# Kernel optimization log

Measured on AMD Instinct MI355X. Metric: run time of the kernel, lower is better.

## Reference

```python
import jax, jax.numpy as jnp
import numpy as np

L, B, E, H = 1024, 8, 1024, 16
HD = E // H
SCALE = HD ** -0.5
EPS = 1e-5


def setup_inputs() -> dict:
    key = jax.random.key(0)
    ks = jax.random.split(key, 6)
    s = E ** -0.5
    return {
        "x": jax.random.normal(ks[0], (L, B, E), dtype=jnp.float32),
        "attn_mask": jnp.zeros((L, L), dtype=jnp.float32),
        "Wq": jax.random.normal(ks[1], (E, E), dtype=jnp.float32) * s,
        "bq": jnp.zeros((E,), dtype=jnp.float32),
        "Wk": jax.random.normal(ks[2], (E, E), dtype=jnp.float32) * s,
        "bk": jnp.zeros((E,), dtype=jnp.float32),
        "Wv": jax.random.normal(ks[3], (E, E), dtype=jnp.float32) * s,
        "bv": jnp.zeros((E,), dtype=jnp.float32),
        "Wo": jax.random.normal(ks[4], (E, E), dtype=jnp.float32) * s,
        "bo": jnp.zeros((E,), dtype=jnp.float32),
        "gamma": jnp.ones((E,), dtype=jnp.float32),
        "beta": jnp.zeros((E,), dtype=jnp.float32),
    }


def _layernorm(x, gamma, beta):
    mu = jnp.mean(x, axis=-1, keepdims=True)
    var = jnp.mean(jnp.square(x - mu), axis=-1, keepdims=True)
    return (x - mu) * jax.lax.rsqrt(var + EPS) * gamma + beta


def reference(x, attn_mask, Wq, bq, Wk, bk, Wv, bv, Wo, bo, gamma, beta):
    # x: (L, B, E); pre-LN residual attention block (dropout=0, eval)
    ln_x = _layernorm(x, gamma, beta)
    # torch Linear: y = x @ W.T + b
    q = (ln_x @ Wq.T + bq) * SCALE
    k = ln_x @ Wk.T + bk
    v = ln_x @ Wv.T + bv
    # (L, B, E) -> (B, H, L, hd)
    def split_heads(t):
        return t.reshape(L, B, H, HD).transpose(1, 2, 0, 3)
    q, k, v = split_heads(q), split_heads(k), split_heads(v)
    # full attention matrix, as in the original non-fused bmm path
    attn = jnp.einsum('bhqd,bhkd->bhqk', q, k) + attn_mask[None, None]
    attn = jax.nn.softmax(attn, axis=-1)
    out = jnp.einsum('bhqk,bhkd->bhqd', attn, v)  # (B, H, L, hd)
    out = out.transpose(2, 0, 1, 3).reshape(L, B, E)
    out = out @ Wo.T + bo
    return x + out
```

## Files before the change

kernel.cpp:

```cpp
#include <hip/hip_runtime.h>

#define LL 1024
#define BB 8
#define EE 1024
#define HH 16
#define HD 64
#define MROWS (LL*BB)

typedef __attribute__((ext_vector_type(8))) short short8v;
typedef __attribute__((ext_vector_type(4))) float f32x4;
typedef __attribute__((ext_vector_type(16))) float f32x16;

#define LOG2E 1.44269504088896f

__device__ __forceinline__ unsigned short tobf(float f) {
    union { float f; unsigned u; } un; un.f = f;
    unsigned u = un.u;
    u += 0x7fffu + ((u >> 16) & 1u);
    return (unsigned short)(u >> 16);
}

__device__ __forceinline__ float max3f(float a, float b, float c) {
    return fmaxf(fmaxf(a, b), c);
}

__device__ __forceinline__ void load_lds16(const unsigned short* g, unsigned short* l) {
    __builtin_amdgcn_global_load_lds((const __attribute__((address_space(1))) unsigned int*)g,
                                     (__attribute__((address_space(3))) unsigned int*)l,
                                     16, 0, 0);
}

__global__ __launch_bounds__(256) void convw4_kernel(const float* __restrict__ w0,
                                                     const float* __restrict__ w1,
                                                     const float* __restrict__ w2,
                                                     const float* __restrict__ w3,
                                                     unsigned short* __restrict__ o0,
                                                     unsigned short* __restrict__ o1,
                                                     unsigned short* __restrict__ o2,
                                                     unsigned short* __restrict__ o3) {
    const float* w; unsigned short* o;
    switch (blockIdx.y) {
        case 0:  w = w0; o = o0; break;
        case 1:  w = w1; o = o1; break;
        case 2:  w = w2; o = o2; break;
        default: w = w3; o = o3; break;
    }
    int i = (blockIdx.x * 256 + threadIdx.x) * 4;
    float4 v = *(const float4*)&w[i];
    ushort4 r;
    r.x = tobf(v.x); r.y = tobf(v.y); r.z = tobf(v.z); r.w = tobf(v.w);
    *(ushort4*)&o[i] = r;
}

__global__ __launch_bounds__(256) void ln_kernel(const float* __restrict__ x,
                                                 const float* __restrict__ gamma,
                                                 const float* __restrict__ beta,
                                                 unsigned short* __restrict__ out) {
    const int row = blockIdx.x;
    const int tid = threadIdx.x;
    const float4 v = *(const float4*)&x[(size_t)row * EE + tid * 4];
    float s = v.x + v.y + v.z + v.w;
    float q = v.x*v.x + v.y*v.y + v.z*v.z + v.w*v.w;
    #pragma unroll
    for (int off = 1; off < 64; off <<= 1) {
        s += __shfl_xor(s, off);
        q += __shfl_xor(q, off);
    }
    __shared__ float ss[4], sq[4];
    const int wv = tid >> 6;
    if ((tid & 63) == 0) { ss[wv] = s; sq[wv] = q; }
    __syncthreads();
    s = ss[0] + ss[1] + ss[2] + ss[3];
    q = sq[0] + sq[1] + sq[2] + sq[3];
    const float mu = s * (1.0f / EE);
    const float var = q * (1.0f / EE) - mu * mu;
    const float rs = rsqrtf(var + 1e-5f);
    ushort4 o;
    o.x = tobf((v.x - mu) * rs * gamma[tid*4+0] + beta[tid*4+0]);
    o.y = tobf((v.y - mu) * rs * gamma[tid*4+1] + beta[tid*4+1]);
    o.z = tobf((v.z - mu) * rs * gamma[tid*4+2] + beta[tid*4+2]);
    o.w = tobf((v.w - mu) * rs * gamma[tid*4+3] + beta[tid*4+3]);
    *(ushort4*)&out[(size_t)row * EE + tid * 4] = o;
}

#define GEMM128_BODY(A_, W_)                                                              \
    __shared__ unsigned short a_sh[128*64];                                               \
    __shared__ unsigned short b_sh[128*64];                                               \
    const int tid = threadIdx.x, lane = tid & 63, wave = tid >> 6;                        \
    const int bm = blockIdx.y * 128, bn = blockIdx.x * 128;                               \
    const int wr = (wave >> 1) * 64, wc = (wave & 1) * 64;                                \
    const int l16 = lane & 15, q4 = lane >> 4;                                            \
    const int grow8 = lane >> 3;                                                          \
    const int gsl = ((lane & 7) ^ grow8) * 8;                                             \
    f32x4 acc[4][4] = {};                                                                 \
    for (int k0 = 0; k0 < EE; k0 += 64) {                                                 \
        _Pragma("unroll")                                                                 \
        for (int i = 0; i < 4; ++i) {                                                     \
            const int ch = wave * 4 + i;                                                  \
            load_lds16(&A_[(size_t)(bm + ch*8 + grow8)*EE + k0 + gsl], a_sh + ch*512);    \
            load_lds16(&W_[(size_t)(bn + ch*8 + grow8)*EE + k0 + gsl], b_sh + ch*512);    \
        }                                                                                 \
        __syncthreads();                                                                  \
        _Pragma("unroll")                                                                 \
        for (int kh = 0; kh < 2; ++kh) {                                                  \
            short8v af[4], bf[4];                                                         \
            _Pragma("unroll")                                                             \
            for (int mi = 0; mi < 4; ++mi)                                                \
                af[mi] = *(const short8v*)((const char*)a_sh                              \
                           + (size_t)(wr + mi*16 + l16)*128 + (((kh*4 + q4) ^ (l16 & 7))*16)); \
            _Pragma("unroll")                                                             \
            for (int ni = 0; ni < 4; ++ni)                                                \
                bf[ni] = *(const short8v*)((const char*)b_sh                              \
                           + (size_t)(wc + ni*16 + l16)*128 + (((kh*4 + q4) ^ (l16 & 7))*16)); \
            _Pragma("unroll")                                                             \
            for (int mi = 0; mi < 4; ++mi)                                                \
                _Pragma("unroll")                                                         \
                for (int ni = 0; ni < 4; ++ni)                                            \
                    acc[mi][ni] = __builtin_amdgcn_mfma_f32_16x16x32_bf16(af[mi], bf[ni], acc[mi][ni], 0, 0, 0); \
        }                                                                                 \
        __syncthreads();                                                                  \
    }

__global__ __launch_bounds__(256) void gemm_qkv(const unsigned short* __restrict__ A,
                                                const unsigned short* __restrict__ W,
                                                const float* __restrict__ bq,
                                                const float* __restrict__ bk,
                                                const float* __restrict__ bv,
                                                unsigned short* __restrict__ qo,
                                                unsigned short* __restrict__ ko,
                                                unsigned short* __restrict__ vo) {
    GEMM128_BODY(A, W)
    const int seg = blockIdx.x >> 3;
    const float* bias = seg == 0 ? bq : (seg == 1 ? bk : bv);
    #pragma unroll
    for (int mi = 0; mi < 4; ++mi) {
        #pragma unroll
        for (int ni = 0; ni < 4; ++ni) {
            #pragma unroll
            for (int r = 0; r < 4; ++r) {
                const int m  = bm + wr + mi*16 + (lane >> 4)*4 + r;
                const int nn = (bn & 1023) + wc + ni*16 + l16;
                const float v = acc[mi][ni][r] + bias[nn];
                const int l = m >> 3, b = m & 7, h = nn >> 6, d = nn & 63;
                if (seg == 0)      qo[((size_t)(b*HH + h) * LL + l) * HD + d] = tobf(v * (0.125f * LOG2E));
                else if (seg == 1) ko[((size_t)(b*HH + h) * LL + l) * HD + d] = tobf(v);
                else               vo[((size_t)(b*HH + h) * HD + d) * LL + l] = tobf(v);
            }
        }
    }
}

__global__ __launch_bounds__(256) void gemm_o(const unsigned short* __restrict__ A,
                                              const unsigned short* __restrict__ W,
                                              const float* __restrict__ bias,
                                              const float* __restrict__ xres,
                                              float* __restrict__ outf) {
    GEMM128_BODY(A, W)
    #pragma unroll
    for (int mi = 0; mi < 4; ++mi) {
        #pragma unroll
        for (int ni = 0; ni < 4; ++ni) {
            #pragma unroll
            for (int r = 0; r < 4; ++r) {
                const int m = bm + wr + mi*16 + (lane >> 4)*4 + r;
                const int n = bn + wc + ni*16 + l16;
                outf[(size_t)m * EE + n] = acc[mi][ni][r] + bias[n] + xres[(size_t)m * EE + n];
            }
        }
    }
}

__global__ __launch_bounds__(256) void attn_kernel(const unsigned short* __restrict__ qarr,
                                                   const unsigned short* __restrict__ karr,
                                                   const unsigned short* __restrict__ vtarr,
                                                   const float* __restrict__ mask,
                                                   unsigned short* __restrict__ attn_out) {
    __shared__ __attribute__((aligned(16))) unsigned short k_sh[2][64*64];
    __shared__ __attribute__((aligned(16))) unsigned short v_sh[2][64*64];
    const int tid = threadIdx.x, lane = tid & 63, wave = tid >> 6;
    const int l32 = lane & 31, hi = lane >> 5;
    const int bh = blockIdx.y;
    const int qtok = blockIdx.x * 128 + wave * 32 + l32;
    const unsigned short* qb = qarr  + (size_t)bh * LL * HD;
    const unsigned short* kb = karr  + (size_t)bh * LL * HD;
    const unsigned short* vb = vtarr + (size_t)bh * HD * LL;

    short8v qf[4];
    #pragma unroll
    for (int dc = 0; dc < 4; ++dc)
        qf[dc] = *(const short8v*)&qb[(size_t)qtok * HD + dc*16 + hi*8];

    f32x16 acc[2] = {};
    float mrun = -1e30f, srun = 0.f;

    auto stage = [&](int buf, int kv) {
        #pragma unroll
        for (int i = 0; i < 2; ++i) {
            const int r = wave*16 + i*8 + (lane >> 3);
            const int c = ((lane & 7) ^ (r & 7)) * 8;
            load_lds16(&kb[(size_t)(kv + r) * HD + c], &k_sh[buf][(wave*16 + i*8) * 64]);
            load_lds16(&vb[(size_t)r * LL + kv + c],   &v_sh[buf][(wave*16 + i*8) * 64]);
        }
    };

    const float* mbase = &mask[(size_t)qtok * LL + hi*4];
    float4 mcur[4], mnxt[4];
    #pragma unroll
    for (int g = 0; g < 4; ++g) mcur[g] = *(const float4*)&mbase[g*8];

    stage(0, 0);
    for (int t = 0; t < LL/64; ++t) {
        const int buf = t & 1;
        __syncthreads();
        if (t < LL/64 - 1) stage(buf ^ 1, (t + 1) * 64);

        #pragma unroll
        for (int sub = 0; sub < 2; ++sub) {
            {
                const int nt = (sub == 0) ? t : (t < LL/64 - 1 ? t + 1 : t);
                const int ns = sub ^ 1;
                const float* mrow = &mbase[(size_t)nt*64 + ns*32];
                #pragma unroll
                for (int g = 0; g < 4; ++g) mnxt[g] = *(const float4*)&mrow[g*8];
            }
            f32x16 s = {};
            __builtin_amdgcn_s_setprio(1);
            #pragma unroll
            for (int dc = 0; dc < 4; ++dc) {
                const int row = sub*32 + l32;
                const short8v kf = *(const short8v*)((const char*)&k_sh[buf][0]
                                     + (size_t)row*128 + (((dc*2 + hi) ^ (l32 & 7)) * 16));
                s = __builtin_amdgcn_mfma_f32_32x32x16_bf16(kf, qf[dc], s, 0, 0, 0);
            }
            __builtin_amdgcn_s_setprio(0);
            #pragma unroll
            for (int g = 0; g < 4; ++g) {
                s[4*g+0] = fmaf(mcur[g].x, LOG2E, s[4*g+0]);
                s[4*g+1] = fmaf(mcur[g].y, LOG2E, s[4*g+1]);
                s[4*g+2] = fmaf(mcur[g].z, LOG2E, s[4*g+2]);
                s[4*g+3] = fmaf(mcur[g].w, LOG2E, s[4*g+3]);
            }
            #pragma unroll
            for (int g = 0; g < 4; ++g) mcur[g] = mnxt[g];
            const float a0 = max3f(s[0],  s[1],  s[2]);
            const float a1 = max3f(s[3],  s[4],  s[5]);
            const float a2 = max3f(s[6],  s[7],  s[8]);
            const float a3 = max3f(s[9],  s[10], s[11]);
            const float a4 = max3f(s[12], s[13], s[14]);
            float pm = fmaxf(max3f(a0, a1, a2), max3f(a3, a4, s[15]));
            pm = fmaxf(pm, __shfl_xor(pm, 32));
            if (__any(pm - mrun > 8.0f)) {
                const float mn = fmaxf(mrun, pm);
                const float al = exp2f(mrun - mn);
                #pragma unroll
                for (int i = 0; i < 16; ++i) { acc[0][i] *= al; acc[1][i] *= al; }
                srun *= al;
                mrun = mn;
            }
            float p[16];
            #pragma unroll
            for (int i = 0; i < 16; ++i) p[i] = exp2f(s[i] - mrun);
            const float t0 = p[0]+p[1],   t1 = p[2]+p[3],   t2 = p[4]+p[5],   t3 = p[6]+p[7];
            const float t4 = p[8]+p[9],   t5 = p[10]+p[11], t6 = p[12]+p[13], t7 = p[14]+p[15];
            const float u0 = t0+t1, u1 = t2+t3, u2 = t4+t5, u3 = t6+t7;
            float rs = (u0+u1) + (u2+u3);
            rs += __shfl_xor(rs, 32);
            srun += rs;
            unsigned w[8];
            #pragma unroll
            for (int j = 0; j < 8; ++j)
                asm("v_cvt_pk_bf16_f32 %0, %1, %2" : "=v"(w[j]) : "v"(p[2*j]), "v"(p[2*j+1]));
            asm volatile("v_permlane32_swap_b32 %0, %1" : "+v"(w[0]), "+v"(w[2]));
            asm volatile("v_permlane32_swap_b32 %0, %1" : "+v"(w[1]), "+v"(w[3]));
            asm volatile("v_permlane32_swap_b32 %0, %1" : "+v"(w[4]), "+v"(w[6]));
            asm volatile("v_permlane32_swap_b32 %0, %1" : "+v"(w[5]), "+v"(w[7]));
            union { uint4 u; short8v s8; } pb0, pb1;
            pb0.u = make_uint4(w[0], w[1], w[2], w[3]);
            pb1.u = make_uint4(w[4], w[5], w[6], w[7]);
            __builtin_amdgcn_s_setprio(1);
            #pragma unroll
            for (int dt = 0; dt < 2; ++dt) {
                const int row = dt*32 + l32;
                const short8v vf0 = *(const short8v*)((const char*)&v_sh[buf][0]
                                      + (size_t)row*128 + ((((sub*2+0)*2 + hi) ^ (l32 & 7)) * 16));
                const short8v vf1 = *(const short8v*)((const char*)&v_sh[buf][0]
                                      + (size_t)row*128 + ((((sub*2+1)*2 + hi) ^ (l32 & 7)) * 16));
                acc[dt] = __builtin_amdgcn_mfma_f32_32x32x16_bf16(vf0, pb0.s8, acc[dt], 0, 0, 0);
                acc[dt] = __builtin_amdgcn_mfma_f32_32x32x16_bf16(vf1, pb1.s8, acc[dt], 0, 0, 0);
            }
            __builtin_amdgcn_s_setprio(0);
        }
    }
    const float inv = 1.0f / srun;
    const int b = bh >> 4, h = bh & 15;
    unsigned short* orow = attn_out + ((size_t)qtok * BB + b) * EE + h * HD;
    #pragma unroll
    for (int dt = 0; dt < 2; ++dt) {
        #pragma unroll
        for (int g = 0; g < 4; ++g) {
            const float a0 = acc[dt][4*g+0]*inv, a1 = acc[dt][4*g+1]*inv;
            const float a2 = acc[dt][4*g+2]*inv, a3 = acc[dt][4*g+3]*inv;
            unsigned lo, hw;
            asm("v_cvt_pk_bf16_f32 %0, %1, %2" : "=v"(lo) : "v"(a0), "v"(a1));
            asm("v_cvt_pk_bf16_f32 %0, %1, %2" : "=v"(hw) : "v"(a2), "v"(a3));
            *(uint2*)&orow[dt*32 + g*8 + hi*4] = make_uint2(lo, hw);
        }
    }
}

extern "C" void kernel_launch(void* const* d_in, const int* in_sizes, int n_in,
                              void* d_out, int out_size, void* d_ws, size_t ws_size,
                              hipStream_t stream) {
    (void)in_sizes; (void)n_in; (void)out_size; (void)ws_size;
    const float* x     = (const float*)d_in[0];
    const float* mask  = (const float*)d_in[1];
    const float* Wq    = (const float*)d_in[2];
    const float* bq    = (const float*)d_in[3];
    const float* Wk    = (const float*)d_in[4];
    const float* bk    = (const float*)d_in[5];
    const float* Wv    = (const float*)d_in[6];
    const float* bv    = (const float*)d_in[7];
    const float* Wo    = (const float*)d_in[8];
    const float* bo    = (const float*)d_in[9];
    const float* gamma = (const float*)d_in[10];
    const float* beta  = (const float*)d_in[11];
    float* out = (float*)d_out;

    unsigned short* ws   = (unsigned short*)d_ws;
    unsigned short* ln   = ws;
    unsigned short* wqkv = ln   + (size_t)MROWS * EE;
    unsigned short* wob  = wqkv + (size_t)3 * EE * EE;
    unsigned short* qb   = wob  + (size_t)EE * EE;
    unsigned short* kbp  = qb   + (size_t)BB * HH * LL * HD;
    unsigned short* vtb  = kbp  + (size_t)BB * HH * LL * HD;
    unsigned short* attnb = ln;

    convw4_kernel<<<dim3(1024, 4), 256, 0, stream>>>(
        Wq, Wk, Wv, Wo,
        wqkv, wqkv + (size_t)EE * EE, wqkv + (size_t)2 * EE * EE, wob);
    ln_kernel<<<MROWS, 256, 0, stream>>>(x, gamma, beta, ln);

    gemm_qkv<<<dim3(24, 64), 256, 0, stream>>>(ln, wqkv, bq, bk, bv, qb, kbp, vtb);

    attn_kernel<<<dim3(LL / 128, BB * HH), 256, 0, stream>>>(qb, kbp, vtb, mask, attnb);

    gemm_o<<<dim3(8, 64), 256, 0, stream>>>(attnb, wob, bo, x, out);
}
```

Baseline: 228.9 us.

## Double-buffer GEMM K-tiles and batch both QK^T sub-tiles before softmax

The shared GEMM body now uses a K step of 32 with two LDS buffers, prefetching the next tile while MFMAs run on the current one, and drops the XOR swizzle in favour of a plain row layout. The attention loop now issues all eight QK^T MFMAs for both 32-key halves up front, then runs softmax and PV on each half through a shared lambda. Mask prefetch across iterations is replaced by loads within the iteration. The unswizzled LDS layout may cause bank conflicts, and holding two score tiles raises register pressure.

```diff
diff --git a/kernel.cpp b/kernel.cpp
--- a/kernel.cpp
+++ b/kernel.cpp
@@ -84,40 +84,41 @@
 }
 
 #define GEMM128_BODY(A_, W_)                                                              \
-    __shared__ unsigned short a_sh[128*64];                                               \
-    __shared__ unsigned short b_sh[128*64];                                               \
+    __shared__ unsigned short a_sh[2][128*32];                                            \
+    __shared__ unsigned short b_sh[2][128*32];                                            \
     const int tid = threadIdx.x, lane = tid & 63, wave = tid >> 6;                        \
     const int bm = blockIdx.y * 128, bn = blockIdx.x * 128;                               \
     const int wr = (wave >> 1) * 64, wc = (wave & 1) * 64;                                \
-    const int l16 = lane & 15, q4 = lane >> 4;                                            \
-    const int grow8 = lane >> 3;                                                          \
-    const int gsl = ((lane & 7) ^ grow8) * 8;                                             \
+    const int l16 = lane & 15, lk8 = (lane >> 4) * 8;                                     \
+    const int grow = lane >> 2, gcol = (lane & 3) * 8;                                    \
     f32x4 acc[4][4] = {};                                                                 \
-    for (int k0 = 0; k0 < EE; k0 += 64) {                                                 \
+    _Pragma("unroll")                                                                     \
+    for (int i = 0; i < 2; ++i) {                                                         \
+        const int ch = wave * 2 + i;                                                      \
+        load_lds16(&A_[(size_t)(bm + ch*16 + grow)*EE + gcol], &a_sh[0][ch*512]);         \
+        load_lds16(&W_[(size_t)(bn + ch*16 + grow)*EE + gcol], &b_sh[0][ch*512]);         \
+    }                                                                                     \
+    __syncthreads();                                                                      \
+    for (int k0 = 0; k0 < EE; k0 += 32) {                                                 \
+        const int cur = (k0 >> 5) & 1;                                                    \
+        if (k0 + 32 < EE) {                                                               \
+            _Pragma("unroll")                                                             \
+            for (int i = 0; i < 2; ++i) {                                                 \
+                const int ch = wave * 2 + i;                                              \
+                load_lds16(&A_[(size_t)(bm + ch*16 + grow)*EE + k0 + 32 + gcol], &a_sh[cur^1][ch*512]); \
+                load_lds16(&W_[(size_t)(bn + ch*16 + grow)*EE + k0 + 32 + gcol], &b_sh[cur^1][ch*512]); \
+            }                                                                             \
+        }                                                                                 \
+        short8v af[4], bf[4];                                                             \
         _Pragma("unroll")                                                                 \
-        for (int i = 0; i < 4; ++i) {                                                     \
-            const int ch = wave * 4 + i;                                                  \
-            load_lds16(&A_[(size_t)(bm + ch*8 + grow8)*EE + k0 + gsl], a_sh + ch*512);    \
-            load_lds16(&W_[(size_t)(bn + ch*8 + grow8)*EE + k0 + gsl], b_sh + ch*512);    \
-        }                                                                                 \
-        __syncthreads();                                                                  \
+        for (int mi = 0; mi < 4; ++mi) af[mi] = *(const short8v*)&a_sh[cur][(wr + mi*16 + l16)*32 + lk8]; \
         _Pragma("unroll")                                                                 \
-        for (int kh = 0; kh < 2; ++kh) {                                                  \
-            short8v af[4], bf[4];                                                         \
-            _Pragma("unroll")                                                             \
-            for (int mi = 0; mi < 4; ++mi)                                                \
-                af[mi] = *(const short8v*)((const char*)a_sh                              \
-                           + (size_t)(wr + mi*16 + l16)*128 + (((kh*4 + q4) ^ (l16 & 7))*16)); \
+        for (int ni = 0; ni < 4; ++ni) bf[ni] = *(const short8v*)&b_sh[cur][(wc + ni*16 + l16)*32 + lk8]; \
+        _Pragma("unroll")                                                                 \
+        for (int mi = 0; mi < 4; ++mi)                                                    \
             _Pragma("unroll")                                                             \
             for (int ni = 0; ni < 4; ++ni)                                                \
-                bf[ni] = *(const short8v*)((const char*)b_sh                              \
-                           + (size_t)(wc + ni*16 + l16)*128 + (((kh*4 + q4) ^ (l16 & 7))*16)); \
-            _Pragma("unroll")                                                             \
-            for (int mi = 0; mi < 4; ++mi)                                                \
-                _Pragma("unroll")                                                         \
-                for (int ni = 0; ni < 4; ++ni)                                            \
-                    acc[mi][ni] = __builtin_amdgcn_mfma_f32_16x16x32_bf16(af[mi], bf[ni], acc[mi][ni], 0, 0, 0); \
-        }                                                                                 \
+                acc[mi][ni] = __builtin_amdgcn_mfma_f32_16x16x32_bf16(af[mi], bf[ni], acc[mi][ni], 0, 0, 0); \
         __syncthreads();                                                                  \
     }
 
@@ -203,93 +204,99 @@
         }
     };
 
+    auto finish = [&](f32x16& s, const float4* mreg, int sub, int buf) {
+        #pragma unroll
+        for (int g = 0; g < 4; ++g) {
+            s[4*g+0] = fmaf(mreg[g].x, LOG2E, s[4*g+0]);
+            s[4*g+1] = fmaf(mreg[g].y, LOG2E, s[4*g+1]);
+            s[4*g+2] = fmaf(mreg[g].z, LOG2E, s[4*g+2]);
+            s[4*g+3] = fmaf(mreg[g].w, LOG2E, s[4*g+3]);
+        }
+        const float a0 = max3f(s[0],  s[1],  s[2]);
+        const float a1 = max3f(s[3],  s[4],  s[5]);
+        const float a2 = max3f(s[6],  s[7],  s[8]);
+        const float a3 = max3f(s[9],  s[10], s[11]);
+        const float a4 = max3f(s[12], s[13], s[14]);
+        float pm = fmaxf(max3f(a0, a1, a2), max3f(a3, a4, s[15]));
+        pm = fmaxf(pm, __shfl_xor(pm, 32));
+        if (__any(pm - mrun > 8.0f)) {
+            const float mn = fmaxf(mrun, pm);
+            const float al = exp2f(mrun - mn);
+            #pragma unroll
+            for (int i = 0; i < 16; ++i) { acc[0][i] *= al; acc[1][i] *= al; }
+            srun *= al;
+            mrun = mn;
+        }
+        float p[16];
+        #pragma unroll
+        for (int i = 0; i < 16; ++i) p[i] = exp2f(s[i] - mrun);
+        const float t0 = p[0]+p[1],   t1 = p[2]+p[3],   t2 = p[4]+p[5],   t3 = p[6]+p[7];
+        const float t4 = p[8]+p[9],   t5 = p[10]+p[11], t6 = p[12]+p[13], t7 = p[14]+p[15];
+        const float u0 = t0+t1, u1 = t2+t3, u2 = t4+t5, u3 = t6+t7;
+        float rs = (u0+u1) + (u2+u3);
+        rs += __shfl_xor(rs, 32);
+        srun += rs;
+        unsigned w[8];
+        #pragma unroll
+        for (int j = 0; j < 8; ++j)
+            asm("v_cvt_pk_bf16_f32 %0, %1, %2" : "=v"(w[j]) : "v"(p[2*j]), "v"(p[2*j+1]));
+        asm volatile("v_permlane32_swap_b32 %0, %1" : "+v"(w[0]), "+v"(w[2]));
+        asm volatile("v_permlane32_swap_b32 %0, %1" : "+v"(w[1]), "+v"(w[3]));
+        asm volatile("v_permlane32_swap_b32 %0, %1" : "+v"(w[4]), "+v"(w[6]));
+        asm volatile("v_permlane32_swap_b32 %0, %1" : "+v"(w[5]), "+v"(w[7]));
+        union { uint4 u; short8v s8; } pb0, pb1;
+        pb0.u = make_uint4(w[0], w[1], w[2], w[3]);
+        pb1.u = make_uint4(w[4], w[5], w[6], w[7]);
+        __builtin_amdgcn_s_setprio(1);
+        #pragma unroll
+        for (int dt = 0; dt < 2; ++dt) {
+            const int row = dt*32 + l32;
+            const short8v vf0 = *(const short8v*)((const char*)&v_sh[buf][0]
+                                  + (size_t)row*128 + ((((sub*2+0)*2 + hi) ^ (l32 & 7)) * 16));
+            const short8v vf1 = *(const short8v*)((const char*)&v_sh[buf][0]
+                                  + (size_t)row*128 + ((((sub*2+1)*2 + hi) ^ (l32 & 7)) * 16));
+            acc[dt] = __builtin_amdgcn_mfma_f32_32x32x16_bf16(vf0, pb0.s8, acc[dt], 0, 0, 0);
+            acc[dt] = __builtin_amdgcn_mfma_f32_32x32x16_bf16(vf1, pb1.s8, acc[dt], 0, 0, 0);
+        }
+        __builtin_amdgcn_s_setprio(0);
+    };
+
     const float* mbase = &mask[(size_t)qtok * LL + hi*4];
-    float4 mcur[4], mnxt[4];
-    #pragma unroll
-    for (int g = 0; g < 4; ++g) mcur[g] = *(const float4*)&mbase[g*8];
-
     stage(0, 0);
-    for (int t = 0; t < LL/64; ++t) {
+    const int NT = LL / 64;
+    for (int t = 0; t < NT; ++t) {
         const int buf = t & 1;
         __syncthreads();
-        if (t < LL/64 - 1) stage(buf ^ 1, (t + 1) * 64);
-
-        #pragma unroll
-        for (int sub = 0; sub < 2; ++sub) {
-            {
-                const int nt = (sub == 0) ? t : (t < LL/64 - 1 ? t + 1 : t);
-                const int ns = sub ^ 1;
-                const float* mrow = &mbase[(size_t)nt*64 + ns*32];
-                #pragma unroll
-                for (int g = 0; g < 4; ++g) mnxt[g] = *(const float4*)&mrow[g*8];
-            }
-            f32x16 s = {};
-            __builtin_amdgcn_s_setprio(1);
-            #pragma unroll
-            for (int dc = 0; dc < 4; ++dc) {
-                const int row = sub*32 + l32;
-                const short8v kf = *(const short8v*)((const char*)&k_sh[buf][0]
-                                     + (size_t)row*128 + (((dc*2 + hi) ^ (l32 & 7)) * 16));
-                s = __builtin_amdgcn_mfma_f32_32x32x16_bf16(kf, qf[dc], s, 0, 0, 0);
-            }
-            __builtin_amdgcn_s_setprio(0);
-            #pragma unroll
-            for (int g = 0; g < 4; ++g) {
-                s[4*g+0] = fmaf(mcur[g].x, LOG2E, s[4*g+0]);
-                s[4*g+1] = fmaf(mcur[g].y, LOG2E, s[4*g+1]);
-                s[4*g+2] = fmaf(mcur[g].z, LOG2E, s[4*g+2]);
-                s[4*g+3] = fmaf(mcur[g].w, LOG2E, s[4*g+3]);
-            }
-            #pragma unroll
-            for (int g = 0; g < 4; ++g) mcur[g] = mnxt[g];
-            const float a0 = max3f(s[0],  s[1],  s[2]);
-            const float a1 = max3f(s[3],  s[4],  s[5]);
-            const float a2 = max3f(s[6],  s[7],  s[8]);
-            const float a3 = max3f(s[9],  s[10], s[11]);
-            const float a4 = max3f(s[12], s[13], s[14]);
-            float pm = fmaxf(max3f(a0, a1, a2), max3f(a3, a4, s[15]));
-            pm = fmaxf(pm, __shfl_xor(pm, 32));
-            if (__any(pm - mrun > 8.0f)) {
-                const float mn = fmaxf(mrun, pm);
-                const float al = exp2f(mrun - mn);
-                #pragma unroll
-                for (int i = 0; i < 16; ++i) { acc[0][i] *= al; acc[1][i] *= al; }
-                srun *= al;
-                mrun = mn;
-            }
-            float p[16];
-            #pragma unroll
-            for (int i = 0; i < 16; ++i) p[i] = exp2f(s[i] - mrun);
-            const float t0 = p[0]+p[1],   t1 = p[2]+p[3],   t2 = p[4]+p[5],   t3 = p[6]+p[7];
-            const float t4 = p[8]+p[9],   t5 = p[10]+p[11], t6 = p[12]+p[13], t7 = p[14]+p[15];
-            const float u0 = t0+t1, u1 = t2+t3, u2 = t4+t5, u3 = t6+t7;
-            float rs = (u0+u1) + (u2+u3);
-            rs += __shfl_xor(rs, 32);
-            srun += rs;
-            unsigned w[8];
-            #pragma unroll
-            for (int j = 0; j < 8; ++j)
-                asm("v_cvt_pk_bf16_f32 %0, %1, %2" : "=v"(w[j]) : "v"(p[2*j]), "v"(p[2*j+1]));
-            asm volatile("v_permlane32_swap_b32 %0, %1" : "+v"(w[0]), "+v"(w[2]));
-            asm volatile("v_permlane32_swap_b32 %0, %1" : "+v"(w[1]), "+v"(w[3]));
-            asm volatile("v_permlane32_swap_b32 %0, %1" : "+v"(w[4]), "+v"(w[6]));
-            asm volatile("v_permlane32_swap_b32 %0, %1" : "+v"(w[5]), "+v"(w[7]));
-            union { uint4 u; short8v s8; } pb0, pb1;
-            pb0.u = make_uint4(w[0], w[1], w[2], w[3]);
-            pb1.u = make_uint4(w[4], w[5], w[6], w[7]);
-            __builtin_amdgcn_s_setprio(1);
-            #pragma unroll
-            for (int dt = 0; dt < 2; ++dt) {
-                const int row = dt*32 + l32;
-                const short8v vf0 = *(const short8v*)((const char*)&v_sh[buf][0]
-                                      + (size_t)row*128 + ((((sub*2+0)*2 + hi) ^ (l32 & 7)) * 16));
-                const short8v vf1 = *(const short8v*)((const char*)&v_sh[buf][0]
-                                      + (size_t)row*128 + ((((sub*2+1)*2 + hi) ^ (l32 & 7)) * 16));
-                acc[dt] = __builtin_amdgcn_mfma_f32_32x32x16_bf16(vf0, pb0.s8, acc[dt], 0, 0, 0);
-                acc[dt] = __builtin_amdgcn_mfma_f32_32x32x16_bf16(vf1, pb1.s8, acc[dt], 0, 0, 0);
-            }
-            __builtin_amdgcn_s_setprio(0);
-        }
+        if (t < NT - 1) stage(buf ^ 1, (t + 1) * 64);
+
+        float4 m0[4], m1[4];
+        {
+            const float* mrow = &mbase[(size_t)t * 64];
+            #pragma unroll
+            for (int g = 0; g < 4; ++g) m0[g] = *(const float4*)&mrow[g*8];
+        }
+        f32x16 s0 = {}, s1 = {};
+        __builtin_amdgcn_s_setprio(1);
+        #pragma unroll
+        for (int dc = 0; dc < 4; ++dc) {
+            const short8v kf = *(const short8v*)((const char*)&k_sh[buf][0]
+                                 + (size_t)(l32)*128 + (((dc*2 + hi) ^ (l32 & 7)) * 16));
+            s0 = __builtin_amdgcn_mfma_f32_32x32x16_bf16(kf, qf[dc], s0, 0, 0, 0);
+        }
+        #pragma unroll
+        for (int dc = 0; dc < 4; ++dc) {
+            const short8v kf = *(const short8v*)((const char*)&k_sh[buf][0]
+                                 + (size_t)(32 + l32)*128 + (((dc*2 + hi) ^ (l32 & 7)) * 16));
+            s1 = __builtin_amdgcn_mfma_f32_32x32x16_bf16(kf, qf[dc], s1, 0, 0, 0);
+        }
+        __builtin_amdgcn_s_setprio(0);
+        {
+            const float* mrow = &mbase[(size_t)t * 64 + 32];
+            #pragma unroll
+            for (int g = 0; g < 4; ++g) m1[g] = *(const float4*)&mrow[g*8];
+        }
+        finish(s0, m0, 0, buf);
+        finish(s1, m1, 1, buf);
     }
     const float inv = 1.0f / srun;
     const int b = bh >> 4, h = bh & 15;
```

Result: slower. 238.8 us (+4.3%).
